# Performance work log

Measured on AMD Instinct MI355X. Metric: run time of the kernel, lower is better.

## Reference

```python
import jax, jax.numpy as jnp
import numpy as np

B, S, D, H = 2, 2048, 1024, 16
HD = D // H                 # head_dim = 64
BLOCK = 16                  # _DEFAULT_BLOCK_SIZE
NB = S // BLOCK             # max_blocks_per_seq = 128
WINDOW = 512
NEG = jnp.float32(-1e30)


def setup_inputs() -> dict:
    key = jax.random.key(0)
    ks = jax.random.split(key, 5)
    x = jax.random.normal(ks[0], (B, S, D), jnp.float32)
    scale = D ** -0.5
    wq = jax.random.normal(ks[1], (D, D), jnp.float32) * scale
    wk = jax.random.normal(ks[2], (D, D), jnp.float32) * scale
    wv = jax.random.normal(ks[3], (D, D), jnp.float32) * scale
    wo = jax.random.normal(ks[4], (D, D), jnp.float32) * scale
    # sequential paged layout (matches the module's synthesized-cache fallback)
    block_tables = jnp.arange(B * NB, dtype=jnp.int32).reshape(B, NB)
    slot_mapping = jnp.arange(B * S, dtype=jnp.int32)
    context_lens = jnp.full((B,), S, dtype=jnp.int32)
    return {"x": x, "wq": wq, "wk": wk, "wv": wv, "wo": wo,
            "block_tables": block_tables, "slot_mapping": slot_mapping,
            "context_lens": context_lens, "window_size": WINDOW}


def reference(x, wq, wk, wv, wo, block_tables, slot_mapping, context_lens, window_size):
    b, s, d = x.shape
    # Q/K/V projections (nn.Linear, bias=False: y = x @ W^T)
    q = (x @ wq.T).reshape(b, s, H, HD)
    k = (x @ wk.T).reshape(b, s, H, HD)
    v = (x @ wv.T).reshape(b, s, H, HD)

    # ---- memopt_C.write_cache: scatter K/V into the physical slot pool ----
    num_slots = b * s
    key_cache = jnp.zeros((num_slots, H, HD), x.dtype).at[slot_mapping].set(k.reshape(-1, H, HD))
    value_cache = jnp.zeros((num_slots, H, HD), x.dtype).at[slot_mapping].set(v.reshape(-1, H, HD))

    # ---- dynamic_sparse_attention: read KV through block_tables ----
    t = jnp.arange(s)
    # physical slot of logical token t of sequence b: block_tables[b, t//BLOCK]*BLOCK + t%BLOCK
    slots = block_tables[:, t // BLOCK].astype(jnp.int32) * BLOCK + (t % BLOCK)[None, :].astype(jnp.int32)  # [B,S]
    kc = key_cache[slots]    # [B,S,H,HD]
    vc = value_cache[slots]  # [B,S,H,HD]

    scores = jnp.einsum('bqhd,bkhd->bhqk', q, kc) * (HD ** -0.5)  # [B,H,S,S]
    qpos = t[:, None]
    kpos = t[None, :]
    # causal + window-limited visibility (window_size tokens of history)
    vis = (kpos <= qpos) & (qpos - kpos < window_size)            # [S,S]
    ctx = t[None, :] < context_lens[:, None]                       # [B,S]
    mask = vis[None, None, :, :] & ctx[:, None, None, :]
    scores = jnp.where(mask, scores, NEG)
    attn = jax.nn.softmax(scores, axis=-1)
    out = jnp.einsum('bhqk,bkhd->bqhd', attn, vc).reshape(b, s, d)
    return out @ wo.T
```

## Files before the change

### kernel.cpp

```cpp
#include <hip/hip_runtime.h>

typedef __attribute__((ext_vector_type(4))) float  f32x4;
typedef __attribute__((ext_vector_type(8))) short  bf16x8;

typedef __attribute__((address_space(3))) void lds_void_t;
typedef __attribute__((address_space(1))) void g_void_t;

#define S_LEN  2048
#define DMODEL 1024
#define NHEAD  16
#define HDIM   64
#define NBLK   128
#define BATCH  2
#define KT     64
#define VP     72

__device__ __forceinline__ short f2bf(float f) {
  union { float f; unsigned u; } v; v.f = f;
  unsigned r = v.u + 0x7fffu + ((v.u >> 16) & 1u);
  return (short)(r >> 16);
}

__global__ __launch_bounds__(256) void cvt_all_kernel(
    const float* __restrict__ x,  const float* __restrict__ wq,
    const float* __restrict__ wk, const float* __restrict__ wv,
    const float* __restrict__ wo,
    short* __restrict__ xb,  short* __restrict__ wqb,
    short* __restrict__ wkb, short* __restrict__ wvb,
    short* __restrict__ wob) {
  const long i = ((long)blockIdx.x * 256 + threadIdx.x) * 8;
  const float* s; short* d; long off;
  if (i < 4194304L)      { s = x;  d = xb;  off = i; }
  else if (i < 5242880L) { s = wq; d = wqb; off = i - 4194304L; }
  else if (i < 6291456L) { s = wk; d = wkb; off = i - 5242880L; }
  else if (i < 7340032L) { s = wv; d = wvb; off = i - 6291456L; }
  else                   { s = wo; d = wob; off = i - 7340032L; }
  f32x4 a = *(const f32x4*)(s + off);
  f32x4 b = *(const f32x4*)(s + off + 4);
  bf16x8 o;
  o[0]=f2bf(a[0]); o[1]=f2bf(a[1]); o[2]=f2bf(a[2]); o[3]=f2bf(a[3]);
  o[4]=f2bf(b[0]); o[5]=f2bf(b[1]); o[6]=f2bf(b[2]); o[7]=f2bf(b[3]);
  *(bf16x8*)(d + off) = o;
}

__global__ __launch_bounds__(256, 2) void gemm8_kernel(
    const short* __restrict__ A,
    const short* __restrict__ W0, const short* __restrict__ W1, const short* __restrict__ W2,
    const int* __restrict__ slot_map,
    short* __restrict__ qbuf, short* __restrict__ kcache, short* __restrict__ vcache)
{
  extern __shared__ short smem[];

  const int bid0 = (int)blockIdx.y * 32 + (int)blockIdx.x;
  const int bid  = (bid0 & 7) * 64 + (bid0 >> 3);
  const int m0 = (bid & 31) * 128;
  const int n0 = (bid >> 5) * 192;
  const short* Ag = A + (size_t)m0 * DMODEL;

  const int tid  = threadIdx.x;
  const int wave = tid >> 6, lane = tid & 63;
  const int l15 = lane & 15, lg = lane >> 4;
  const int wc = wave;
  const int sgs = (tid & 3) ^ ((tid >> 3) & 3);
  const int rg  = (l15 >> 1) & 3;

  f32x4 acc[8][3];
#pragma unroll
  for (int m = 0; m < 8; m++)
#pragma unroll
    for (int n = 0; n < 3; n++) acc[m][n] = (f32x4)0.f;

#define STAGE_A(BUFI, K0, P) {                                                             \
    const int r_ = (((P) * 256 + tid) >> 2);                                               \
    __builtin_amdgcn_global_load_lds(                                                      \
        (g_void_t*)(Ag + (size_t)r_ * DMODEL + (K0) + sgs * 8),                            \
        (lds_void_t*)(smem + (BUFI) * 4096 + ((P) * 256 + tid) * 8), 16, 0, 0); }

#define STAGE_B(BUFI, K0, P) {                                                             \
    const int r_ = (((P) * 256 + tid) >> 2);                                               \
    const int grow = n0 + r_;                                                              \
    const short* wb = (grow < 1024) ? W0 : (grow < 2048) ? W1 : W2;                        \
    __builtin_amdgcn_global_load_lds(                                                      \
        (g_void_t*)(wb + (size_t)(grow & 1023) * DMODEL + (K0) + sgs * 8),                 \
        (lds_void_t*)(smem + 16384 + (BUFI) * 6144 + ((P) * 256 + tid) * 8), 16, 0, 0); }

#define STAGE_TILE(BUFI, K0)                                                               \
    STAGE_A(BUFI, K0, 0); STAGE_A(BUFI, K0, 1);                                            \
    STAGE_B(BUFI, K0, 0); STAGE_B(BUFI, K0, 1); STAGE_B(BUFI, K0, 2);

  const int NT = DMODEL / 32;

  STAGE_TILE(0, 0);
  STAGE_TILE(1, 32);
  STAGE_TILE(2, 64);
  asm volatile("s_waitcnt vmcnt(10)" ::: "memory");
  __builtin_amdgcn_s_barrier();
  asm volatile("" ::: "memory");

  for (int t = 0; t < NT; ++t) {
    const int bi = t & 3;
    if (t + 3 < NT) {
      const int bn = (t + 3) & 3;
      const int kn = (t + 3) * 32;
      STAGE_TILE(bn, kn);
    }
    const short* Ac = smem + bi * 4096;
    const short* Bc = smem + 16384 + bi * 6144;

    bf16x8 af[8], bfr[3];
#pragma unroll
    for (int nt = 0; nt < 3; ++nt) {
      const int row = wc * 48 + nt * 16 + l15;
      bfr[nt] = *(const bf16x8*)(Bc + row * 32 + ((lg ^ rg) << 3));
    }
#pragma unroll
    for (int mi = 0; mi < 8; ++mi) {
      const int row = mi * 16 + l15;
      af[mi] = *(const bf16x8*)(Ac + row * 32 + ((lg ^ rg) << 3));
    }
    __builtin_amdgcn_s_setprio(1);
#pragma unroll
    for (int mi = 0; mi < 8; ++mi)
#pragma unroll
      for (int nt = 0; nt < 3; ++nt)
        acc[mi][nt] = __builtin_amdgcn_mfma_f32_16x16x32_bf16(
            af[mi], bfr[nt], acc[mi][nt], 0, 0, 0);
    __builtin_amdgcn_s_setprio(0);

    if (t < NT - 3)       { asm volatile("s_waitcnt vmcnt(10)" ::: "memory"); }
    else if (t == NT - 3) { asm volatile("s_waitcnt vmcnt(5)"  ::: "memory"); }
    else if (t == NT - 2) { asm volatile("s_waitcnt vmcnt(0)"  ::: "memory"); }
    if (t < NT - 1) {
      asm volatile("" ::: "memory");
      __builtin_amdgcn_s_barrier();
      asm volatile("" ::: "memory");
    }
  }
#undef STAGE_A
#undef STAGE_B
#undef STAGE_TILE

#pragma unroll
  for (int mf = 0; mf < 8; ++mf) {
    const int rowb = m0 + mf * 16 + lg * 4;
#pragma unroll
    for (int r4 = 0; r4 < 4; ++r4) {
      const int row = rowb + r4;
      const int slot = slot_map[row];
#pragma unroll
      for (int nt = 0; nt < 3; ++nt) {
        const int col = n0 + wc * 48 + nt * 16 + l15;
        const short bv = f2bf(acc[mf][nt][r4]);
        if (col < DMODEL)
          qbuf[(size_t)row * DMODEL + col] = bv;
        else if (col < 2 * DMODEL)
          kcache[(size_t)slot * DMODEL + (col - DMODEL)] = bv;
        else
          vcache[(size_t)slot * DMODEL + (col - 2 * DMODEL)] = bv;
      }
    }
  }
}

__global__ __launch_bounds__(256, 2) void gemm1_kernel(
    const short* __restrict__ A, const short* __restrict__ W,
    float* __restrict__ outf)
{
  extern __shared__ short smem1[];

  const int bid0 = (int)blockIdx.y * 32 + (int)blockIdx.x;
  const int bid  = (bid0 & 7) * 32 + (bid0 >> 3);
  const int m0 = (bid & 31) * 128;
  const int n0 = (bid >> 5) * 128;
  const short* Ag = A + (size_t)m0 * DMODEL;
  const short* Bg = W + (size_t)n0 * DMODEL;

  const int tid = threadIdx.x;
  const int wave = tid >> 6, lane = tid & 63;
  const int l15 = lane & 15, lg = lane >> 4;
  const int wr = wave >> 1, wc = wave & 1;
  const int swz = l15 & 7;

  short* const As0 = smem1;
  short* const Bs0 = smem1 + 8192;
  short* const As1 = smem1 + 16384;
  short* const Bs1 = smem1 + 24576;

  f32x4 acc[4][4];
#pragma unroll
  for (int m = 0; m < 4; m++)
#pragma unroll
    for (int n = 0; n < 4; n++) acc[m][n] = (f32x4)0.f;

#define STG1(LA, LB, K0) {                                                                 \
    _Pragma("unroll") for (int p = 0; p < 4; ++p) {                                        \
      const int u = p * 256 + tid; const int r = u >> 3; const int cs = (u & 7) ^ (r & 7); \
      __builtin_amdgcn_global_load_lds((g_void_t*)(Ag + (size_t)r * DMODEL + (K0) + cs * 8), \
          (lds_void_t*)((LA) + (p * 256 + wave * 64) * 8), 16, 0, 0); }                    \
    _Pragma("unroll") for (int p = 0; p < 4; ++p) {                                        \
      const int u = p * 256 + tid; const int r = u >> 3; const int cs = (u & 7) ^ (r & 7); \
      __builtin_amdgcn_global_load_lds((g_void_t*)(Bg + (size_t)r * DMODEL + (K0) + cs * 8), \
          (lds_void_t*)((LB) + (p * 256 + wave * 64) * 8), 16, 0, 0); } }

  STG1(As0, Bs0, 0);
  asm volatile("s_waitcnt vmcnt(0)" ::: "memory");
  __builtin_amdgcn_s_barrier();
  asm volatile("" ::: "memory");

  for (int t = 0; t < 16; ++t) {
    const int cur = t & 1;
    short* const Ac = cur ? As1 : As0;
    short* const Bc = cur ? Bs1 : Bs0;
    short* const An = cur ? As0 : As1;
    short* const Bn = cur ? Bs0 : Bs1;
    if (t + 1 < 16) {
      STG1(An, Bn, (t + 1) * 64);
      asm volatile("s_waitcnt vmcnt(8)" ::: "memory");
    } else {
      asm volatile("s_waitcnt vmcnt(0)" ::: "memory");
    }
    asm volatile("" ::: "memory");
    __builtin_amdgcn_s_barrier();
    asm volatile("" ::: "memory");

    bf16x8 af[4][2], bfr[4][2];
#pragma unroll
    for (int m4 = 0; m4 < 4; ++m4) {
      const int row = wr * 64 + m4 * 16 + l15;
#pragma unroll
      for (int ks = 0; ks < 2; ++ks)
        af[m4][ks] = *(const bf16x8*)(Ac + row * 64 + (((ks * 4 + lg) ^ swz) << 3));
    }
#pragma unroll
    for (int n4 = 0; n4 < 4; ++n4) {
      const int row = wc * 64 + n4 * 16 + l15;
#pragma unroll
      for (int ks = 0; ks < 2; ++ks)
        bfr[n4][ks] = *(const bf16x8*)(Bc + row * 64 + (((ks * 4 + lg) ^ swz) << 3));
    }
    __builtin_amdgcn_s_setprio(1);
#pragma unroll
    for (int m4 = 0; m4 < 4; ++m4)
#pragma unroll
      for (int n4 = 0; n4 < 4; ++n4)
#pragma unroll
        for (int ks = 0; ks < 2; ++ks)
          acc[m4][n4] = __builtin_amdgcn_mfma_f32_16x16x32_bf16(af[m4][ks], bfr[n4][ks], acc[m4][n4], 0, 0, 0);
    __builtin_amdgcn_s_setprio(0);

    asm volatile("" ::: "memory");
    __builtin_amdgcn_s_barrier();
    asm volatile("" ::: "memory");
  }
#undef STG1

#pragma unroll
  for (int m4 = 0; m4 < 4; ++m4) {
    const int rowb = m0 + wr * 64 + m4 * 16 + lg * 4;
#pragma unroll
    for (int n4 = 0; n4 < 4; ++n4) {
      const int col = n0 + wc * 64 + n4 * 16 + l15;
#pragma unroll
      for (int r4 = 0; r4 < 4; ++r4)
        outf[(size_t)(rowb + r4) * DMODEL + col] = acc[m4][n4][r4];
    }
  }
}

__global__ __launch_bounds__(512, 4) void attn_kernel(
    const short* __restrict__ qbuf,
    const short* __restrict__ kcache, const short* __restrict__ vcache,
    const int* __restrict__ block_tables, const int* __restrict__ context_lens,
    const int* __restrict__ window_size,
    short* __restrict__ attn_out)
{
  __shared__ short Ks[KT * 64];
  __shared__ short Vt[HDIM * VP];
  __shared__ short Pb[8 * 16 * VP];

  const int b = blockIdx.z, h = blockIdx.y;
  const int bx = (b & 1) ? ((int)gridDim.x - 1 - (int)blockIdx.x) : (int)blockIdx.x;
  const int q0 = bx * 128;
  const int ctx = context_lens[b];
  const int ws  = window_size[0];
  const int* bt = block_tables + b * NBLK;

  const int tid  = threadIdx.x;
  const int wave = tid >> 6, lane = tid & 63;
  const int l15 = lane & 15, lg = lane >> 4;
  const int qw = q0 + wave * 16;

  const short* qp = qbuf + ((size_t)(b * S_LEN + qw + l15)) * DMODEL + h * HDIM;
  const bf16x8 qf0 = *(const bf16x8*)(qp + lg * 8);
  const bf16x8 qf1 = *(const bf16x8*)(qp + 32 + lg * 8);

  f32x4 oacc[4];
  float lrow[4];
#pragma unroll
  for (int i = 0; i < 4; i++) { oacc[i] = (f32x4)0.f; lrow[i] = 0.f; }

  int kstart = q0 - ws + 1; if (kstart < 0) kstart = 0; kstart &= ~(KT - 1);
  int kend = q0 + 128; if (kend > ctx) kend = ctx;

  const int kr = tid >> 3;
  const int dc = (tid & 7) << 3;
  const float rscale = 0.125f;
  const float FM = 12.f;
  short* pw = Pb + wave * (16 * VP);
  const int swz = (l15 & 7) << 4;

  bf16x8 kreg = (bf16x8)0, vreg = (bf16x8)0;
  {
    const int key = kstart + kr;
    if (key < ctx) {
      const int slot = bt[key >> 4] * 16 + (key & 15);
      kreg = *(const bf16x8*)(kcache + (size_t)slot * DMODEL + h * HDIM + dc);
      vreg = *(const bf16x8*)(vcache + (size_t)slot * DMODEL + h * HDIM + dc);
    }
  }

  for (int kt = kstart; kt < kend; kt += KT) {
    __syncthreads();
    *(bf16x8*)((char*)Ks + kr * 128 + ((dc * 2) ^ ((kr & 7) << 4))) = kreg;
    const int vcol = (kr + dc) & 63;
#pragma unroll
    for (int j = 0; j < 8; j++) Vt[(dc + j) * VP + vcol] = vreg[j];
    kreg = (bf16x8)0; vreg = (bf16x8)0;
    if (kt + KT < kend) {
      const int key = kt + KT + kr;
      if (key < ctx) {
        const int slot = bt[key >> 4] * 16 + (key & 15);
        kreg = *(const bf16x8*)(kcache + (size_t)slot * DMODEL + h * HDIM + dc);
        vreg = *(const bf16x8*)(vcache + (size_t)slot * DMODEL + h * HDIM + dc);
      }
    }
    __syncthreads();

    if ((kt > qw + 15) || (kt + (KT - 1) <= qw - ws)) continue;

    f32x4 sacc[4];
#pragma unroll
    for (int cg = 0; cg < 4; cg++) sacc[cg] = (f32x4)0.f;
#pragma unroll
    for (int cg = 0; cg < 4; cg++) {
      const char* kp = (const char*)Ks + (cg * 16 + l15) * 128;
      const bf16x8 k0 = *(const bf16x8*)(kp + ((lg * 16) ^ swz));
      const bf16x8 k1 = *(const bf16x8*)(kp + ((64 + lg * 16) ^ swz));
      sacc[cg] = __builtin_amdgcn_mfma_f32_16x16x32_bf16(qf0, k0, sacc[cg], 0, 0, 0);
      sacc[cg] = __builtin_amdgcn_mfma_f32_16x16x32_bf16(qf1, k1, sacc[cg], 0, 0, 0);
    }

    const bool fullvis = (kt + (KT - 1) <= qw) && (qw + 15 - kt < ws) && (kt + (KT - 1) < ctx);

    if (fullvis) {
#pragma unroll
      for (int r = 0; r < 4; r++) {
        const float e0 = __expf(sacc[0][r] * rscale - FM);
        const float e1 = __expf(sacc[1][r] * rscale - FM);
        const float e2 = __expf(sacc[2][r] * rscale - FM);
        const float e3 = __expf(sacc[3][r] * rscale - FM);
        lrow[r] += (e0 + e1) + (e2 + e3);
        short* pr = pw + (lg * 4 + r) * VP + l15;
        pr[0]  = f2bf(e0); pr[16] = f2bf(e1);
        pr[32] = f2bf(e2); pr[48] = f2bf(e3);
      }
    } else {
#pragma unroll
      for (int r = 0; r < 4; r++) {
        const int qrow = qw + lg * 4 + r;
        const int key0 = kt + l15;
        const bool ok0 = (key0      <= qrow) && (qrow - key0      < ws) && (key0      < ctx);
        const bool ok1 = (key0 + 16 <= qrow) && (qrow - key0 - 16 < ws) && (key0 + 16 < ctx);
        const bool ok2 = (key0 + 32 <= qrow) && (qrow - key0 - 32 < ws) && (key0 + 32 < ctx);
        const bool ok3 = (key0 + 48 <= qrow) && (qrow - key0 - 48 < ws) && (key0 + 48 < ctx);
        const float e0 = ok0 ? __expf(sacc[0][r] * rscale - FM) : 0.f;
        const float e1 = ok1 ? __expf(sacc[1][r] * rscale - FM) : 0.f;
        const float e2 = ok2 ? __expf(sacc[2][r] * rscale - FM) : 0.f;
        const float e3 = ok3 ? __expf(sacc[3][r] * rscale - FM) : 0.f;
        lrow[r] += (e0 + e1) + (e2 + e3);
        short* pr = pw + (lg * 4 + r) * VP + l15;
        pr[0]  = f2bf(e0); pr[16] = f2bf(e1);
        pr[32] = f2bf(e2); pr[48] = f2bf(e3);
      }
    }

    asm volatile("s_waitcnt lgkmcnt(0)" ::: "memory");

#pragma unroll
    for (int kk = 0; kk < 2; kk++) {
      const bf16x8 pa = *(const bf16x8*)(pw + l15 * VP + kk * 32 + lg * 8);
#pragma unroll
      for (int dn = 0; dn < 4; dn++) {
        const int vrow = dn * 16 + l15;
        const int roff = (kk * 32 + lg * 8 + (vrow & ~7)) & 63;
        const bf16x8 vb = *(const bf16x8*)(Vt + vrow * VP + roff);
        oacc[dn] = __builtin_amdgcn_mfma_f32_16x16x32_bf16(pa, vb, oacc[dn], 0, 0, 0);
      }
    }
  }

#pragma unroll
  for (int r = 0; r < 4; r++) {
    float ls = lrow[r];
    ls += __shfl_xor(ls, 1); ls += __shfl_xor(ls, 2);
    ls += __shfl_xor(ls, 4); ls += __shfl_xor(ls, 8);
    const float inv = 1.f / fmaxf(ls, 1e-30f);
    const int row = qw + lg * 4 + r;
    short* op = attn_out + ((size_t)(b * S_LEN + row)) * DMODEL + h * HDIM;
#pragma unroll
    for (int dn = 0; dn < 4; dn++)
      op[dn * 16 + l15] = f2bf(oacc[dn][r] * inv);
  }
}

extern "C" void kernel_launch(void* const* d_in, const int* in_sizes, int n_in,
                              void* d_out, int out_size, void* d_ws, size_t ws_size,
                              hipStream_t stream) {
  const float* x  = (const float*)d_in[0];
  const float* wq = (const float*)d_in[1];
  const float* wk = (const float*)d_in[2];
  const float* wv = (const float*)d_in[3];
  const float* wo = (const float*)d_in[4];
  const int* block_tables = (const int*)d_in[5];
  const int* slot_mapping = (const int*)d_in[6];
  const int* context_lens = (const int*)d_in[7];
  const int* window_size  = (const int*)d_in[8];
  float* out = (float*)d_out;

  char* ws = (char*)d_ws;
  short* xb     = (short*)(ws + (size_t)( 0 << 20));
  short* wqb    = (short*)(ws + (size_t)( 8 << 20));
  short* wkb    = (short*)(ws + (size_t)(10 << 20));
  short* wvb    = (short*)(ws + (size_t)(12 << 20));
  short* wob    = (short*)(ws + (size_t)(14 << 20));
  short* qbuf   = (short*)(ws + (size_t)(16 << 20));
  short* kcache = (short*)(ws + (size_t)(24 << 20));
  short* vcache = (short*)(ws + (size_t)(32 << 20));
  short* abuf   = (short*)(ws + (size_t)(40 << 20));

  static bool ginit = [] {
    hipFuncSetAttribute(reinterpret_cast<const void*>(&gemm8_kernel),
                        hipFuncAttributeMaxDynamicSharedMemorySize, 81920);
    hipFuncSetAttribute(reinterpret_cast<const void*>(&gemm1_kernel),
                        hipFuncAttributeMaxDynamicSharedMemorySize, 65536);
    return true;
  }();
  (void)ginit;

  cvt_all_kernel<<<4096, 256, 0, stream>>>(x, wq, wk, wv, wo, xb, wqb, wkb, wvb, wob);

  gemm8_kernel<<<dim3(32, 16), 256, 81920, stream>>>(xb, wqb, wkb, wvb, slot_mapping,
                                                     qbuf, kcache, vcache);

  attn_kernel<<<dim3(S_LEN / 128, NHEAD, BATCH), 512, 0, stream>>>(
      qbuf, kcache, vcache, block_tables, context_lens, window_size, abuf);

  gemm1_kernel<<<dim3(32, 8), 256, 65536, stream>>>(abuf, wob, out);
}
```

Measured before the change: 97.79 us.

## Rework QKV GEMM into 256x256 tiles with 8 waves and split-phase pipeline

```diff
diff --git a/kernel.cpp b/kernel.cpp
--- a/kernel.cpp
+++ b/kernel.cpp
@@ -43,7 +43,7 @@
   *(bf16x8*)(d + off) = o;
 }
 
-__global__ __launch_bounds__(256, 2) void gemm8_kernel(
+__global__ __launch_bounds__(512, 2) void gemm8_kernel(
     const short* __restrict__ A,
     const short* __restrict__ W0, const short* __restrict__ W1, const short* __restrict__ W2,
     const int* __restrict__ slot_map,
@@ -51,113 +51,158 @@
 {
   extern __shared__ short smem[];
 
-  const int bid0 = (int)blockIdx.y * 32 + (int)blockIdx.x;
-  const int bid  = (bid0 & 7) * 64 + (bid0 >> 3);
-  const int m0 = (bid & 31) * 128;
-  const int n0 = (bid >> 5) * 192;
+  const int bid0 = (int)blockIdx.y * 16 + (int)blockIdx.x;
+  const int bid  = (bid0 & 7) * 24 + (bid0 >> 3);
+  const int m0 = (bid & 15) * 256;
+  const int n0 = (bid >> 4) * 256;
+  const int wsel = n0 >> 10;
+  const short* W = (wsel == 0) ? W0 : (wsel == 1) ? W1 : W2;
   const short* Ag = A + (size_t)m0 * DMODEL;
+  const short* Bg = W + (size_t)(n0 & 1023) * DMODEL;
 
   const int tid  = threadIdx.x;
   const int wave = tid >> 6, lane = tid & 63;
   const int l15 = lane & 15, lg = lane >> 4;
-  const int wc = wave;
-  const int sgs = (tid & 3) ^ ((tid >> 3) & 3);
-  const int rg  = (l15 >> 1) & 3;
-
-  f32x4 acc[8][3];
+  const int wr = wave >> 2, wc = wave & 3;
+  const int swz = l15 & 7;
+
+  short* const A0s = smem;
+  short* const A1s = smem + 16384;
+  short* const B0s = smem + 32768;
+  short* const B1s = smem + 49152;
+
+  f32x4 acc[8][4];
 #pragma unroll
   for (int m = 0; m < 8; m++)
 #pragma unroll
-    for (int n = 0; n < 3; n++) acc[m][n] = (f32x4)0.f;
-
-#define STAGE_A(BUFI, K0, P) {                                                             \
-    const int r_ = (((P) * 256 + tid) >> 2);                                               \
-    __builtin_amdgcn_global_load_lds(                                                      \
-        (g_void_t*)(Ag + (size_t)r_ * DMODEL + (K0) + sgs * 8),                            \
-        (lds_void_t*)(smem + (BUFI) * 4096 + ((P) * 256 + tid) * 8), 16, 0, 0); }
-
-#define STAGE_B(BUFI, K0, P) {                                                             \
-    const int r_ = (((P) * 256 + tid) >> 2);                                               \
-    const int grow = n0 + r_;                                                              \
-    const short* wb = (grow < 1024) ? W0 : (grow < 2048) ? W1 : W2;                        \
-    __builtin_amdgcn_global_load_lds(                                                      \
-        (g_void_t*)(wb + (size_t)(grow & 1023) * DMODEL + (K0) + sgs * 8),                 \
-        (lds_void_t*)(smem + 16384 + (BUFI) * 6144 + ((P) * 256 + tid) * 8), 16, 0, 0); }
-
-#define STAGE_TILE(BUFI, K0)                                                               \
-    STAGE_A(BUFI, K0, 0); STAGE_A(BUFI, K0, 1);                                            \
-    STAGE_B(BUFI, K0, 0); STAGE_B(BUFI, K0, 1); STAGE_B(BUFI, K0, 2);
-
-  const int NT = DMODEL / 32;
-
-  STAGE_TILE(0, 0);
-  STAGE_TILE(1, 32);
-  STAGE_TILE(2, 64);
-  asm volatile("s_waitcnt vmcnt(10)" ::: "memory");
-  __builtin_amdgcn_s_barrier();
-  asm volatile("" ::: "memory");
-
-  for (int t = 0; t < NT; ++t) {
-    const int bi = t & 3;
-    if (t + 3 < NT) {
-      const int bn = (t + 3) & 3;
-      const int kn = (t + 3) * 32;
-      STAGE_TILE(bn, kn);
-    }
-    const short* Ac = smem + bi * 4096;
-    const short* Bc = smem + 16384 + bi * 6144;
-
-    bf16x8 af[8], bfr[3];
-#pragma unroll
-    for (int nt = 0; nt < 3; ++nt) {
-      const int row = wc * 48 + nt * 16 + l15;
-      bfr[nt] = *(const bf16x8*)(Bc + row * 32 + ((lg ^ rg) << 3));
-    }
-#pragma unroll
-    for (int mi = 0; mi < 8; ++mi) {
-      const int row = mi * 16 + l15;
-      af[mi] = *(const bf16x8*)(Ac + row * 32 + ((lg ^ rg) << 3));
-    }
-    __builtin_amdgcn_s_setprio(1);
-#pragma unroll
-    for (int mi = 0; mi < 8; ++mi)
-#pragma unroll
-      for (int nt = 0; nt < 3; ++nt)
-        acc[mi][nt] = __builtin_amdgcn_mfma_f32_16x16x32_bf16(
-            af[mi], bfr[nt], acc[mi][nt], 0, 0, 0);
+    for (int n = 0; n < 4; n++) acc[m][n] = (f32x4)0.f;
+
+#define STG_A(DST, K0, P) {                                                                \
+    const int g_ = (P) * 512 + tid;                                                        \
+    const int r_ = g_ >> 3;                                                                \
+    const int cs_ = (g_ & 7) ^ (r_ & 7);                                                   \
+    __builtin_amdgcn_global_load_lds((g_void_t*)(Ag + (size_t)r_ * DMODEL + (K0) + cs_ * 8), \
+        (lds_void_t*)((DST) + ((P) * 512 + wave * 64) * 8), 16, 0, 0); }
+
+#define STG_B(DST, K0, P) {                                                                \
+    const int g_ = (P) * 512 + tid;                                                        \
+    const int r_ = g_ >> 3;                                                                \
+    const int cs_ = (g_ & 7) ^ (r_ & 7);                                                   \
+    __builtin_amdgcn_global_load_lds((g_void_t*)(Bg + (size_t)r_ * DMODEL + (K0) + cs_ * 8), \
+        (lds_void_t*)((DST) + ((P) * 512 + wave * 64) * 8), 16, 0, 0); }
+
+#define BAR() do { asm volatile("" ::: "memory");                \
+    __builtin_amdgcn_s_barrier();                                \
+    asm volatile("" ::: "memory"); } while (0)
+
+#define LGKM0() asm volatile("s_waitcnt lgkmcnt(0)" ::: "memory")
+
+#define RD_A(DEST, BUF, MH)                                                                \
+    _Pragma("unroll") for (int mi = 0; mi < 4; ++mi) {                                     \
+      const int row = wr * 128 + (MH) * 64 + mi * 16 + l15;                                \
+      _Pragma("unroll") for (int ks = 0; ks < 2; ++ks)                                     \
+        DEST[mi][ks] = *(const bf16x8*)((BUF) + row * 64 + (((ks * 4 + lg) ^ swz) << 3)); }
+
+#define RD_B(DEST, BUF, NH)                                                                \
+    _Pragma("unroll") for (int ni = 0; ni < 2; ++ni) {                                     \
+      const int row = wc * 64 + (NH) * 32 + ni * 16 + l15;                                 \
+      _Pragma("unroll") for (int ks = 0; ks < 2; ++ks)                                     \
+        DEST[ni][ks] = *(const bf16x8*)((BUF) + row * 64 + (((ks * 4 + lg) ^ swz) << 3)); }
+
+#define MMA(MH, NH, AF, BF)                                                                \
+    __builtin_amdgcn_s_setprio(1);                                                         \
+    _Pragma("unroll") for (int mi = 0; mi < 4; ++mi)                                       \
+    _Pragma("unroll") for (int ni = 0; ni < 2; ++ni)                                       \
+    _Pragma("unroll") for (int ks = 0; ks < 2; ++ks)                                       \
+      acc[(MH) * 4 + mi][(NH) * 2 + ni] = __builtin_amdgcn_mfma_f32_16x16x32_bf16(         \
+          AF[mi][ks], BF[ni][ks], acc[(MH) * 4 + mi][(NH) * 2 + ni], 0, 0, 0);             \
     __builtin_amdgcn_s_setprio(0);
 
-    if (t < NT - 3)       { asm volatile("s_waitcnt vmcnt(10)" ::: "memory"); }
-    else if (t == NT - 3) { asm volatile("s_waitcnt vmcnt(5)"  ::: "memory"); }
-    else if (t == NT - 2) { asm volatile("s_waitcnt vmcnt(0)"  ::: "memory"); }
-    if (t < NT - 1) {
-      asm volatile("" ::: "memory");
-      __builtin_amdgcn_s_barrier();
-      asm volatile("" ::: "memory");
-    }
-  }
-#undef STAGE_A
-#undef STAGE_B
-#undef STAGE_TILE
-
+  STG_A(A0s, 0, 0); STG_A(A0s, 0, 1); STG_A(A0s, 0, 2); STG_A(A0s, 0, 3);
+  STG_B(B0s, 0, 0); STG_B(B0s, 0, 1); STG_B(B0s, 0, 2); STG_B(B0s, 0, 3);
+  STG_A(A1s, 64, 0); STG_A(A1s, 64, 1);
+  asm volatile("s_waitcnt vmcnt(2)" ::: "memory");
+  BAR();
+
+  const int NI = DMODEL / 128;
+  for (int i = 0; i < NI; ++i) {
+    const int K0 = i * 128;
+    const bool lst = (i == NI - 1);
+    bf16x8 af0[4][2], af1[4][2], bf0[2][2], bf1[2][2];
+
+    RD_A(af0, A0s, 0); RD_B(bf0, B0s, 0);
+    STG_A(A1s, K0 + 64, 2); STG_A(A1s, K0 + 64, 3);
+    BAR(); LGKM0();
+    MMA(0, 0, af0, bf0);
+    BAR();
+
+    RD_B(bf1, B0s, 1);
+    STG_B(B1s, K0 + 64, 0); STG_B(B1s, K0 + 64, 1);
+    BAR(); LGKM0();
+    MMA(0, 1, af0, bf1);
+    BAR();
+
+    RD_A(af1, A0s, 1);
+    STG_B(B1s, K0 + 64, 2); STG_B(B1s, K0 + 64, 3);
+    BAR(); LGKM0();
+    MMA(1, 0, af1, bf0);
+    BAR();
+
+    if (!lst) { STG_A(A0s, K0 + 128, 0); STG_A(A0s, K0 + 128, 1); }
+    MMA(1, 1, af1, bf1);
+    if (!lst) { asm volatile("s_waitcnt vmcnt(2)" ::: "memory"); }
+    else      { asm volatile("s_waitcnt vmcnt(0)" ::: "memory"); }
+    BAR();
+
+    RD_A(af0, A1s, 0); RD_B(bf0, B1s, 0);
+    if (!lst) { STG_A(A0s, K0 + 128, 2); STG_A(A0s, K0 + 128, 3); }
+    BAR(); LGKM0();
+    MMA(0, 0, af0, bf0);
+    BAR();
+
+    RD_B(bf1, B1s, 1);
+    if (!lst) { STG_B(B0s, K0 + 128, 0); STG_B(B0s, K0 + 128, 1); }
+    BAR(); LGKM0();
+    MMA(0, 1, af0, bf1);
+    BAR();
+
+    RD_A(af1, A1s, 1);
+    if (!lst) { STG_B(B0s, K0 + 128, 2); STG_B(B0s, K0 + 128, 3); }
+    BAR(); LGKM0();
+    MMA(1, 0, af1, bf0);
+    BAR();
+
+    if (!lst) { STG_A(A1s, K0 + 192, 0); STG_A(A1s, K0 + 192, 1); }
+    MMA(1, 1, af1, bf1);
+    if (!lst) {
+      asm volatile("s_waitcnt vmcnt(2)" ::: "memory");
+      BAR();
+    }
+  }
+#undef STG_A
+#undef STG_B
+#undef BAR
+#undef LGKM0
+#undef RD_A
+#undef RD_B
+#undef MMA
+
+  const int colb = (n0 & 1023) + wc * 64;
 #pragma unroll
   for (int mf = 0; mf < 8; ++mf) {
-    const int rowb = m0 + mf * 16 + lg * 4;
+    const int rowb = m0 + wr * 128 + mf * 16 + lg * 4;
 #pragma unroll
     for (int r4 = 0; r4 < 4; ++r4) {
       const int row = rowb + r4;
-      const int slot = slot_map[row];
-#pragma unroll
-      for (int nt = 0; nt < 3; ++nt) {
-        const int col = n0 + wc * 48 + nt * 16 + l15;
-        const short bv = f2bf(acc[mf][nt][r4]);
-        if (col < DMODEL)
-          qbuf[(size_t)row * DMODEL + col] = bv;
-        else if (col < 2 * DMODEL)
-          kcache[(size_t)slot * DMODEL + (col - DMODEL)] = bv;
-        else
-          vcache[(size_t)slot * DMODEL + (col - 2 * DMODEL)] = bv;
+      short* base;
+      if (wsel == 0) base = qbuf + (size_t)row * DMODEL;
+      else {
+        const int slot = slot_map[row];
+        base = ((wsel == 1) ? kcache : vcache) + (size_t)slot * DMODEL;
       }
+#pragma unroll
+      for (int nf = 0; nf < 4; ++nf)
+        base[colb + nf * 16 + l15] = f2bf(acc[mf][nf][r4]);
     }
   }
 }
@@ -440,7 +485,7 @@
 
   static bool ginit = [] {
     hipFuncSetAttribute(reinterpret_cast<const void*>(&gemm8_kernel),
-                        hipFuncAttributeMaxDynamicSharedMemorySize, 81920);
+                        hipFuncAttributeMaxDynamicSharedMemorySize, 131072);
     hipFuncSetAttribute(reinterpret_cast<const void*>(&gemm1_kernel),
                         hipFuncAttributeMaxDynamicSharedMemorySize, 65536);
     return true;
@@ -449,8 +494,8 @@
 
   cvt_all_kernel<<<4096, 256, 0, stream>>>(x, wq, wk, wv, wo, xb, wqb, wkb, wvb, wob);
 
-  gemm8_kernel<<<dim3(32, 16), 256, 81920, stream>>>(xb, wqb, wkb, wvb, slot_mapping,
-                                                     qbuf, kcache, vcache);
+  gemm8_kernel<<<dim3(16, 12), 512, 131072, stream>>>(xb, wqb, wkb, wvb, slot_mapping,
+                                                      qbuf, kcache, vcache);
 
   attn_kernel<<<dim3(S_LEN / 128, NHEAD, BATCH), 512, 0, stream>>>(
       qbuf, kcache, vcache, block_tables, context_lens, window_size, abuf);
```

Result: faster. 89.84 us (median of 2 runs) (-8.1%).

## Restructure QKV GEMM to 256x192 tiles with 8 waves and interleaved staging

Applied to the files above, without the earlier changes.

```diff
diff --git a/kernel.cpp b/kernel.cpp
--- a/kernel.cpp
+++ b/kernel.cpp
@@ -43,7 +43,7 @@
   *(bf16x8*)(d + off) = o;
 }
 
-__global__ __launch_bounds__(256, 2) void gemm8_kernel(
+__global__ __launch_bounds__(512, 2) void gemm8_kernel(
     const short* __restrict__ A,
     const short* __restrict__ W0, const short* __restrict__ W1, const short* __restrict__ W2,
     const int* __restrict__ slot_map,
@@ -51,18 +51,17 @@
 {
   extern __shared__ short smem[];
 
-  const int bid0 = (int)blockIdx.y * 32 + (int)blockIdx.x;
-  const int bid  = (bid0 & 7) * 64 + (bid0 >> 3);
-  const int m0 = (bid & 31) * 128;
-  const int n0 = (bid >> 5) * 192;
+  const int bid0 = (int)blockIdx.y * 16 + (int)blockIdx.x;
+  const int bid  = (bid0 & 7) * 32 + (bid0 >> 3);
+  const int m0 = (bid & 15) * 256;
+  const int n0 = (bid >> 4) * 192;
   const short* Ag = A + (size_t)m0 * DMODEL;
 
   const int tid  = threadIdx.x;
   const int wave = tid >> 6, lane = tid & 63;
   const int l15 = lane & 15, lg = lane >> 4;
-  const int wc = wave;
-  const int sgs = (tid & 3) ^ ((tid >> 3) & 3);
-  const int rg  = (l15 >> 1) & 3;
+  const int wr = wave >> 2, wc = wave & 3;
+  const int swz = l15 & 7;
 
   f32x4 acc[8][3];
 #pragma unroll
@@ -70,79 +69,106 @@
 #pragma unroll
     for (int n = 0; n < 3; n++) acc[m][n] = (f32x4)0.f;
 
-#define STAGE_A(BUFI, K0, P) {                                                             \
-    const int r_ = (((P) * 256 + tid) >> 2);                                               \
-    __builtin_amdgcn_global_load_lds(                                                      \
-        (g_void_t*)(Ag + (size_t)r_ * DMODEL + (K0) + sgs * 8),                            \
-        (lds_void_t*)(smem + (BUFI) * 4096 + ((P) * 256 + tid) * 8), 16, 0, 0); }
-
-#define STAGE_B(BUFI, K0, P) {                                                             \
-    const int r_ = (((P) * 256 + tid) >> 2);                                               \
+#define STG_A(BUFI, K0, P) {                                                               \
+    const int g_ = (P) * 512 + tid;                                                        \
+    const int r_ = g_ >> 3;                                                                \
+    const int cs_ = (g_ & 7) ^ (r_ & 7);                                                   \
+    __builtin_amdgcn_global_load_lds((g_void_t*)(Ag + (size_t)r_ * DMODEL + (K0) + cs_ * 8), \
+        (lds_void_t*)(smem + (BUFI) * 16384 + ((P) * 512 + wave * 64) * 8), 16, 0, 0); }
+
+#define STG_B(BUFI, K0, P) {                                                               \
+    const int g_ = (P) * 512 + tid;                                                        \
+    const int r_ = g_ >> 3;                                                                \
     const int grow = n0 + r_;                                                              \
     const short* wb = (grow < 1024) ? W0 : (grow < 2048) ? W1 : W2;                        \
-    __builtin_amdgcn_global_load_lds(                                                      \
-        (g_void_t*)(wb + (size_t)(grow & 1023) * DMODEL + (K0) + sgs * 8),                 \
-        (lds_void_t*)(smem + 16384 + (BUFI) * 6144 + ((P) * 256 + tid) * 8), 16, 0, 0); }
-
-#define STAGE_TILE(BUFI, K0)                                                               \
-    STAGE_A(BUFI, K0, 0); STAGE_A(BUFI, K0, 1);                                            \
-    STAGE_B(BUFI, K0, 0); STAGE_B(BUFI, K0, 1); STAGE_B(BUFI, K0, 2);
-
-  const int NT = DMODEL / 32;
-
-  STAGE_TILE(0, 0);
-  STAGE_TILE(1, 32);
-  STAGE_TILE(2, 64);
-  asm volatile("s_waitcnt vmcnt(10)" ::: "memory");
-  __builtin_amdgcn_s_barrier();
-  asm volatile("" ::: "memory");
+    const int cs_ = (g_ & 7) ^ (r_ & 7);                                                   \
+    __builtin_amdgcn_global_load_lds((g_void_t*)(wb + (size_t)(grow & 1023) * DMODEL + (K0) + cs_ * 8), \
+        (lds_void_t*)(smem + 49152 + (BUFI) * 12288 + ((P) * 512 + wave * 64) * 8), 16, 0, 0); }
+
+#define BAR() do { asm volatile("" ::: "memory");                \
+    __builtin_amdgcn_s_barrier();                                \
+    asm volatile("" ::: "memory"); } while (0)
+
+#define LGKM0() asm volatile("s_waitcnt lgkmcnt(0)" ::: "memory")
+
+#define RD_B(BUF)                                                                          \
+    _Pragma("unroll") for (int nt = 0; nt < 3; ++nt) {                                     \
+      const int row = wc * 48 + nt * 16 + l15;                                             \
+      _Pragma("unroll") for (int ks = 0; ks < 2; ++ks)                                     \
+        bfr[nt][ks] = *(const bf16x8*)((BUF) + row * 64 + (((ks * 4 + lg) ^ swz) << 3)); }
+
+#define RD_A2(BUF, MQ)                                                                     \
+    _Pragma("unroll") for (int mi = 0; mi < 2; ++mi) {                                     \
+      const int row = wr * 128 + ((MQ) * 2 + mi) * 16 + l15;                               \
+      _Pragma("unroll") for (int ks = 0; ks < 2; ++ks)                                     \
+        af[mi][ks] = *(const bf16x8*)((BUF) + row * 64 + (((ks * 4 + lg) ^ swz) << 3)); }
+
+#define MMA2(MQ)                                                                           \
+    __builtin_amdgcn_s_setprio(1);                                                         \
+    _Pragma("unroll") for (int mi = 0; mi < 2; ++mi)                                       \
+    _Pragma("unroll") for (int nt = 0; nt < 3; ++nt)                                       \
+    _Pragma("unroll") for (int ks = 0; ks < 2; ++ks)                                       \
+      acc[(MQ) * 2 + mi][nt] = __builtin_amdgcn_mfma_f32_16x16x32_bf16(                    \
+          af[mi][ks], bfr[nt][ks], acc[(MQ) * 2 + mi][nt], 0, 0, 0);                       \
+    __builtin_amdgcn_s_setprio(0);
+
+  const int NT = DMODEL / 64;
+
+  STG_A(0, 0, 0); STG_A(0, 0, 1); STG_A(0, 0, 2); STG_A(0, 0, 3);
+  STG_B(0, 0, 0); STG_B(0, 0, 1); STG_B(0, 0, 2);
+  STG_A(1, 64, 0); STG_A(1, 64, 1); STG_A(1, 64, 2); STG_A(1, 64, 3);
+  asm volatile("s_waitcnt vmcnt(4)" ::: "memory");
+  BAR();
 
   for (int t = 0; t < NT; ++t) {
-    const int bi = t & 3;
-    if (t + 3 < NT) {
-      const int bn = (t + 3) & 3;
-      const int kn = (t + 3) * 32;
-      STAGE_TILE(bn, kn);
-    }
-    const short* Ac = smem + bi * 4096;
-    const short* Bc = smem + 16384 + bi * 6144;
-
-    bf16x8 af[8], bfr[3];
-#pragma unroll
-    for (int nt = 0; nt < 3; ++nt) {
-      const int row = wc * 48 + nt * 16 + l15;
-      bfr[nt] = *(const bf16x8*)(Bc + row * 32 + ((lg ^ rg) << 3));
-    }
-#pragma unroll
-    for (int mi = 0; mi < 8; ++mi) {
-      const int row = mi * 16 + l15;
-      af[mi] = *(const bf16x8*)(Ac + row * 32 + ((lg ^ rg) << 3));
-    }
-    __builtin_amdgcn_s_setprio(1);
-#pragma unroll
-    for (int mi = 0; mi < 8; ++mi)
-#pragma unroll
-      for (int nt = 0; nt < 3; ++nt)
-        acc[mi][nt] = __builtin_amdgcn_mfma_f32_16x16x32_bf16(
-            af[mi], bfr[nt], acc[mi][nt], 0, 0, 0);
-    __builtin_amdgcn_s_setprio(0);
-
-    if (t < NT - 3)       { asm volatile("s_waitcnt vmcnt(10)" ::: "memory"); }
-    else if (t == NT - 3) { asm volatile("s_waitcnt vmcnt(5)"  ::: "memory"); }
-    else if (t == NT - 2) { asm volatile("s_waitcnt vmcnt(0)"  ::: "memory"); }
-    if (t < NT - 1) {
-      asm volatile("" ::: "memory");
-      __builtin_amdgcn_s_barrier();
-      asm volatile("" ::: "memory");
-    }
-  }
-#undef STAGE_A
-#undef STAGE_B
-#undef STAGE_TILE
+    const short* Ab = smem + (t % 3) * 16384;
+    const short* Bb = smem + 49152 + (t & 1) * 12288;
+    const int bB = (t + 1) & 1;
+    const int bA = (t + 2) % 3;
+    const int k1 = (t + 1) * 64;
+    const int k2 = (t + 2) * 64;
+    const bool sB = (t + 1 < NT);
+    const bool sA = (t + 2 < NT);
+
+    bf16x8 af[2][2], bfr[3][2];
+
+    RD_B(Bb);
+    RD_A2(Ab, 0);
+    if (sB) { STG_B(bB, k1, 0); }
+    if (sA) { STG_A(bA, k2, 0); }
+    BAR(); LGKM0();
+    MMA2(0);
+
+    RD_A2(Ab, 1);
+    if (sB) { STG_B(bB, k1, 1); }
+    if (sA) { STG_A(bA, k2, 1); }
+    BAR(); LGKM0();
+    MMA2(1);
+
+    RD_A2(Ab, 2);
+    if (sB) { STG_B(bB, k1, 2); }
+    if (sA) { STG_A(bA, k2, 2); }
+    BAR(); LGKM0();
+    MMA2(2);
+
+    RD_A2(Ab, 3);
+    if (sA) { STG_A(bA, k2, 3); }
+    BAR(); LGKM0();
+    MMA2(3);
+    if (t < NT - 2)       { asm volatile("s_waitcnt vmcnt(2)" ::: "memory"); BAR(); }
+    else if (t == NT - 2) { asm volatile("s_waitcnt vmcnt(0)" ::: "memory"); BAR(); }
+  }
+#undef STG_A
+#undef STG_B
+#undef BAR
+#undef LGKM0
+#undef RD_B
+#undef RD_A2
+#undef MMA2
 
 #pragma unroll
   for (int mf = 0; mf < 8; ++mf) {
-    const int rowb = m0 + mf * 16 + lg * 4;
+    const int rowb = m0 + wr * 128 + mf * 16 + lg * 4;
 #pragma unroll
     for (int r4 = 0; r4 < 4; ++r4) {
       const int row = rowb + r4;
@@ -440,7 +466,7 @@
 
   static bool ginit = [] {
     hipFuncSetAttribute(reinterpret_cast<const void*>(&gemm8_kernel),
-                        hipFuncAttributeMaxDynamicSharedMemorySize, 81920);
+                        hipFuncAttributeMaxDynamicSharedMemorySize, 147456);
     hipFuncSetAttribute(reinterpret_cast<const void*>(&gemm1_kernel),
                         hipFuncAttributeMaxDynamicSharedMemorySize, 65536);
     return true;
@@ -449,8 +475,8 @@
 
   cvt_all_kernel<<<4096, 256, 0, stream>>>(x, wq, wk, wv, wo, xb, wqb, wkb, wvb, wob);
 
-  gemm8_kernel<<<dim3(32, 16), 256, 81920, stream>>>(xb, wqb, wkb, wvb, slot_mapping,
-                                                     qbuf, kcache, vcache);
+  gemm8_kernel<<<dim3(16, 16), 512, 147456, stream>>>(xb, wqb, wkb, wvb, slot_mapping,
+                                                      qbuf, kcache, vcache);
 
   attn_kernel<<<dim3(S_LEN / 128, NHEAD, BATCH), 512, 0, stream>>>(
       qbuf, kcache, vcache, block_tables, context_lens, window_size, abuf);
```

New measurement: 90.00 us. 1.09x faster.
